# Performance work log

Hardware: AMD Instinct MI355X
Metric: run time of the kernel (lower is better)

## Reference

```python
import jax, jax.numpy as jnp
import numpy as np

T, B, D, H = 4096, 4, 1024, 8
EPS = 1e-5


def _ln(z, g, b):
    m = jnp.mean(z, axis=-1, keepdims=True)
    v = jnp.mean((z - m) ** 2, axis=-1, keepdims=True)
    return (z - m) * jax.lax.rsqrt(v + EPS) * g + b


def setup_inputs() -> dict:
    key = jax.random.key(0)
    ks = jax.random.split(key, 8)
    s = 0.02
    return {
        "x": jax.random.normal(ks[0], (T, B, D), dtype=jnp.float32),
        "norm_w": jnp.ones((D,), jnp.float32),
        "norm_b": jnp.zeros((D,), jnp.float32),
        "tnorm_w": jnp.ones((D,), jnp.float32),
        "tnorm_b": jnp.zeros((D,), jnp.float32),
        "Wq": jax.random.normal(ks[1], (D, D), jnp.float32) * s,
        "bq": jnp.zeros((D,), jnp.float32),
        "Wk": jax.random.normal(ks[2], (D, D), jnp.float32) * s,
        "bk": jnp.zeros((D,), jnp.float32),
        "Wv": jax.random.normal(ks[3], (D, D), jnp.float32) * s,
        "bv": jnp.zeros((D,), jnp.float32),
    }


def reference(x, norm_w, norm_b, tnorm_w, tnorm_b, Wq, bq, Wk, bk, Wv, bv):
    # x: (T, B, D) -> (B, T, D), matching torch x.permute(1, 0, 2)
    xb = jnp.transpose(x, (1, 0, 2))
    b, t, d = xb.shape
    hd = d // H
    xn = _ln(xb, norm_w, norm_b)          # query branch norm
    xtn = _ln(xb, tnorm_w, tnorm_b)       # key/value branch norm (text_norm applied to x)
    q = (xn @ Wq.T + bq).reshape(b, t, H, hd)
    k = (xtn @ Wk.T + bk).reshape(b, t, H, hd)
    v = (xtn @ Wv.T + bv).reshape(b, t, H, hd)
    q = jax.nn.softmax(q, axis=-1)        # softmax over head-dim
    k = jax.nn.softmax(k, axis=1)         # softmax over time
    # kv state: (B, H, hd, hd)
    att = jnp.einsum('bthd,bthl->bhdl', k, v)
    y = jnp.einsum('bthd,bhdl->bthl', q, att).reshape(b, t, d)
    return y  # original forward returns y directly (proj_out/dropout unused)
```

## Files before the change

kernel.cpp:

```cpp
#include <hip/hip_runtime.h>
#include <cstdint>

#define T_LEN 4096
#define BATCH 4
#define DIM   1024
#define NH    8
#define HDIM  128
#define ROWS  16384

typedef __bf16 bf16x8 __attribute__((ext_vector_type(8)));
typedef float  f32x4  __attribute__((ext_vector_type(4)));

__device__ __forceinline__ unsigned short f2bf(float f) {
  union { float f; unsigned u; } a; a.f = f;
  unsigned u = a.u;
  u += 0x7fff + ((u >> 16) & 1);
  return (unsigned short)(u >> 16);
}
__device__ __forceinline__ float bf2f(unsigned short h) {
  union { unsigned u; float f; } a; a.u = ((unsigned)h) << 16;
  return a.f;
}

__device__ __forceinline__ void gld_lds16(const unsigned short* g, unsigned short* l) {
  __builtin_amdgcn_global_load_lds(
      (const __attribute__((address_space(1))) unsigned int*)g,
      (__attribute__((address_space(3))) unsigned int*)l, 16, 0, 0);
}

__global__ __launch_bounds__(256) void lnw_kernel(
    const float* __restrict__ x, const float* __restrict__ nw, const float* __restrict__ nb,
    const float* __restrict__ tw, const float* __restrict__ tb,
    unsigned short* __restrict__ xn, unsigned short* __restrict__ xtn,
    const float* __restrict__ Wq, const float* __restrict__ Wk, const float* __restrict__ Wv,
    unsigned short* __restrict__ wbf) {
  int tid = threadIdx.x;
  if (blockIdx.x >= ROWS) {
    int i4 = (blockIdx.x - ROWS) * 256 + tid;
    int w = i4 >> 18;
    const float* src = (w == 0) ? Wq : (w == 1 ? Wk : Wv);
    float4 v = ((const float4*)src)[i4 & 262143];
    union { unsigned short u[4]; uint2 d; } o;
    o.u[0] = f2bf(v.x); o.u[1] = f2bf(v.y); o.u[2] = f2bf(v.z); o.u[3] = f2bf(v.w);
    ((uint2*)wbf)[i4] = o.d;
    return;
  }
  int row = blockIdx.x;
  int t = row >> 2, b = row & 3;
  const float4 v = ((const float4*)(x + (size_t)row * DIM))[tid];
  float s  = v.x + v.y + v.z + v.w;
  float s2 = v.x*v.x + v.y*v.y + v.z*v.z + v.w*v.w;
#pragma unroll
  for (int o = 32; o; o >>= 1) { s += __shfl_xor(s, o); s2 += __shfl_xor(s2, o); }
  __shared__ float red[8];
  int wv = tid >> 6;
  if ((tid & 63) == 0) { red[wv] = s; red[4 + wv] = s2; }
  __syncthreads();
  s  = red[0] + red[1] + red[2] + red[3];
  s2 = red[4] + red[5] + red[6] + red[7];
  float mean = s * (1.0f / DIM);
  float var  = s2 * (1.0f / DIM) - mean * mean;
  float rstd = rsqrtf(var + 1e-5f);
  size_t orow = ((size_t)b * T_LEN + t) * DIM;
  int c0 = tid * 4;
  float xv[4] = {v.x, v.y, v.z, v.w};
  union { unsigned short u[4]; uint2 d; } o1, o2;
#pragma unroll
  for (int j = 0; j < 4; ++j) {
    int c = c0 + j;
    float xh = (xv[j] - mean) * rstd;
    o1.u[j] = f2bf(xh * nw[c] + nb[c]);
    o2.u[j] = f2bf(xh * tw[c] + tb[c]);
  }
  *(uint2*)(xn  + orow + c0) = o1.d;
  *(uint2*)(xtn + orow + c0) = o2.d;
}

__global__ __launch_bounds__(512, 4) void kv_gemm(
    const unsigned short* __restrict__ xtn, const unsigned short* __restrict__ wbf,
    const float* __restrict__ bk, const float* __restrict__ bv,
    unsigned short* __restrict__ ko, unsigned short* __restrict__ vo,
    float* __restrict__ Zk) {
  int zz = blockIdx.z + 1;
  const unsigned short* W = wbf + (size_t)zz * DIM * DIM;
  const float* bias = (zz == 1) ? bk : bv;
  unsigned short* outp = (zz == 1) ? ko : vo;

  int m0 = blockIdx.x * 256;
  int n0 = blockIdx.y * 128;

  __shared__ __align__(16) unsigned short lds[24576];

  int tid = threadIdx.x;
  int wave = tid >> 6, lane = tid & 63;
  int wr = wave >> 1, wc = wave & 1;
  int wm = wr * 64, wn = wc * 64;
  int l16 = lane & 15, kq = lane >> 4;
  int rs = (kq ^ ((l16 >> 1) & 3)) * 8;

  int arow = tid >> 2;
  int achk = (tid & 3) ^ ((tid >> 3) & 3);
  const unsigned short* Ag = xtn + (size_t)(m0 + arow) * DIM + achk * 8;
  const unsigned short* Wg = W + (size_t)(n0 + arow) * DIM + achk * 8;

  f32x4 acc[4][4] = {};

  auto stage = [&](int tt, int sb) {
    int kt = tt * 32;
    gld_lds16(Ag + kt,                     lds + sb + wave * 512);
    gld_lds16(Ag + (size_t)128 * DIM + kt, lds + sb + 4096 + wave * 512);
    gld_lds16(Wg + kt,                     lds + sb + 8192 + wave * 512);
  };

  stage(0, 0);
  stage(1, 12288);

  for (int t = 0; t < 32; ++t) {
    int sb = (t & 1) ? 12288 : 0;
    const unsigned short* As = lds + sb;
    const unsigned short* Bs = lds + sb + 8192;

    if (t < 31) asm volatile("s_waitcnt vmcnt(3)" ::: "memory");
    else        asm volatile("s_waitcnt vmcnt(0)" ::: "memory");
    __builtin_amdgcn_sched_barrier(0);
    __builtin_amdgcn_s_barrier();
    __builtin_amdgcn_sched_barrier(0);

    bf16x8 fa[4], fb[4];
#pragma unroll
    for (int i = 0; i < 4; ++i) {
      fa[i] = *(const bf16x8*)(As + (wm + i * 16 + l16) * 32 + rs);
      fb[i] = *(const bf16x8*)(Bs + (wn + i * 16 + l16) * 32 + rs);
    }
#pragma unroll
    for (int i = 0; i < 4; ++i)
#pragma unroll
      for (int j = 0; j < 4; ++j)
        acc[i][j] = __builtin_amdgcn_mfma_f32_16x16x32_bf16(fa[i], fb[j], acc[i][j], 0, 0, 0);

    __builtin_amdgcn_sched_barrier(0);
    __builtin_amdgcn_s_barrier();
    __builtin_amdgcn_sched_barrier(0);
    if (t < 30) stage(t + 2, sb);
    __builtin_amdgcn_sched_barrier(0);
  }

#pragma unroll
  for (int j = 0; j < 4; ++j) {
    float bc = bias[n0 + wn + j * 16 + l16];
#pragma unroll
    for (int i = 0; i < 4; ++i)
#pragma unroll
      for (int r = 0; r < 4; ++r) acc[i][j][r] += bc;
  }

  int b = m0 >> 12;
  int tb = m0 & 4095;
  unsigned short* obase = outp + (size_t)b * DIM * T_LEN + tb;
  bool doExp = (zz == 1);
  float zs[4] = {0.0f, 0.0f, 0.0f, 0.0f};
#pragma unroll
  for (int j = 0; j < 4; ++j) {
    int col = n0 + wn + j * 16 + l16;
    unsigned short* cp = obase + (size_t)col * T_LEN;
#pragma unroll
    for (int i = 0; i < 4; ++i) {
      int t0 = wm + i * 16 + kq * 4;
      union { unsigned short u[4]; uint2 d; } o;
#pragma unroll
      for (int r = 0; r < 4; ++r) {
        float val = acc[i][j][r];
        if (doExp) { val = __expf(val); zs[j] += val; }
        o.u[r] = f2bf(val);
      }
      *(uint2*)(cp + t0) = o.d;
    }
  }
  if (doExp) {
#pragma unroll
    for (int j = 0; j < 4; ++j) {
      zs[j] += __shfl_xor(zs[j], 16);
      zs[j] += __shfl_xor(zs[j], 32);
      if (kq == 0) {
        int col = n0 + wn + j * 16 + l16;
        atomicAdd(Zk + b * DIM + col, zs[j]);
      }
    }
  }
}

__global__ __launch_bounds__(256) void att_gemm(
    const unsigned short* __restrict__ vT, const unsigned short* __restrict__ ksmT,
    float* __restrict__ slabs) {
  int kc = blockIdx.x;
  int bh = blockIdx.y;
  const unsigned short* Arow = vT   + (size_t)bh * HDIM * T_LEN;
  const unsigned short* Brow = ksmT + (size_t)bh * HDIM * T_LEN;
  __shared__ __align__(16) unsigned short As[128 * 64];
  __shared__ __align__(16) unsigned short Bs[128 * 64];
  int tid = threadIdx.x;
  int wave = tid >> 6, lane = tid & 63;
  int wm = (wave >> 1) * 64, wn = (wave & 1) * 64;
  int l16 = lane & 15, kq = lane >> 4;
  int swz = l16 & 7;
  int srow = tid >> 3;
  int skk = (((tid & 7) ^ ((tid >> 3) & 7)) * 8);
  const unsigned short* Ag = Arow + (size_t)srow * T_LEN + skk;
  const unsigned short* Bg = Brow + (size_t)srow * T_LEN + skk;
  unsigned short* Al = As + wave * 512;
  unsigned short* Bl = Bs + wave * 512;
  f32x4 acc[4][4] = {};
  int kbeg = kc * 512;
  for (int kt = kbeg; kt < kbeg + 512; kt += 64) {
#pragma unroll
    for (int p = 0; p < 4; ++p) {
      gld_lds16(Ag + (size_t)(p * 32) * T_LEN + kt, Al + p * 2048);
      gld_lds16(Bg + (size_t)(p * 32) * T_LEN + kt, Bl + p * 2048);
    }
    __syncthreads();
#pragma unroll
    for (int ks4 = 0; ks4 < 2; ++ks4) {
      int coff = (((kq + ks4 * 4) ^ swz) * 8);
      bf16x8 fa[4], fb[4];
#pragma unroll
      for (int i = 0; i < 4; ++i) {
        fa[i] = *(const bf16x8*)(As + (wm + i * 16 + l16) * 64 + coff);
        fb[i] = *(const bf16x8*)(Bs + (wn + i * 16 + l16) * 64 + coff);
      }
#pragma unroll
      for (int i = 0; i < 4; ++i)
#pragma unroll
        for (int j = 0; j < 4; ++j)
          acc[i][j] = __builtin_amdgcn_mfma_f32_16x16x32_bf16(fa[i], fb[j], acc[i][j], 0, 0, 0);
    }
    __syncthreads();
  }
  float* op = slabs + ((size_t)kc * 32 + bh) * 16384;
#pragma unroll
  for (int j = 0; j < 4; ++j) {
    int col = wn + j * 16 + l16;
#pragma unroll
    for (int i = 0; i < 4; ++i) {
      int rb = wm + i * 16 + kq * 4;
#pragma unroll
      for (int r = 0; r < 4; ++r)
        op[(size_t)(rb + r) * 128 + col] = acc[i][j][r];
    }
  }
}

__global__ __launch_bounds__(256) void attcvt(
    const float* __restrict__ slabs, const float* __restrict__ Zk,
    unsigned short* __restrict__ attbf) {
  int idx = blockIdx.x * 256 + threadIdx.x;
  int bh = idx >> 14;
  int b = bh >> 3, h = bh & 7;
  int d = idx & 127;
  float s = 0.0f;
#pragma unroll
  for (int kc = 0; kc < 8; ++kc) s += slabs[(size_t)kc * 524288 + idx];
  float zv = Zk[b * DIM + h * HDIM + d];
  attbf[idx] = f2bf(s / zv);
}

__global__ __launch_bounds__(512) void qy_gemm(
    const unsigned short* __restrict__ xn, const unsigned short* __restrict__ wbf,
    const float* __restrict__ bq, const unsigned short* __restrict__ attbf,
    float* __restrict__ out) {
  int m0 = blockIdx.x * 256;
  int h  = blockIdx.y;
  int n0 = h * HDIM;
  int b  = m0 >> 12;
  int bh = b * 8 + h;

  __shared__ __align__(16) unsigned short lds[24576];

  int tid = threadIdx.x;
  int wave = tid >> 6, lane = tid & 63;
  int wr = wave >> 1, wc = wave & 1;
  int wm = wr * 64, wn = wc * 64;
  int l16 = lane & 15, kq = lane >> 4;
  int rs = (kq ^ ((l16 >> 1) & 3)) * 8;

  int arow = tid >> 2;
  int achk = (tid & 3) ^ ((tid >> 3) & 3);
  const unsigned short* Ag = xn + (size_t)(m0 + arow) * DIM + achk * 8;
  const unsigned short* Wg = wbf + (size_t)(n0 + arow) * DIM + achk * 8;

  f32x4 acc[4][4] = {};

  auto stage = [&](int tt, int sb) {
    int kt = tt * 32;
    gld_lds16(Ag + kt,                     lds + sb + wave * 512);
    gld_lds16(Ag + (size_t)128 * DIM + kt, lds + sb + 4096 + wave * 512);
    gld_lds16(Wg + kt,                     lds + sb + 8192 + wave * 512);
  };

  stage(0, 0);
  stage(1, 12288);

  for (int t = 0; t < 32; ++t) {
    int sb = (t & 1) ? 12288 : 0;
    const unsigned short* As = lds + sb;
    const unsigned short* Bs = lds + sb + 8192;

    if (t < 31) asm volatile("s_waitcnt vmcnt(3)" ::: "memory");
    else        asm volatile("s_waitcnt vmcnt(0)" ::: "memory");
    __builtin_amdgcn_sched_barrier(0);
    __builtin_amdgcn_s_barrier();
    __builtin_amdgcn_sched_barrier(0);

    bf16x8 fa[4], fb[4];
#pragma unroll
    for (int i = 0; i < 4; ++i) {
      fa[i] = *(const bf16x8*)(As + (wm + i * 16 + l16) * 32 + rs);
      fb[i] = *(const bf16x8*)(Bs + (wn + i * 16 + l16) * 32 + rs);
    }
#pragma unroll
    for (int i = 0; i < 4; ++i)
#pragma unroll
      for (int j = 0; j < 4; ++j)
        acc[i][j] = __builtin_amdgcn_mfma_f32_16x16x32_bf16(fa[i], fb[j], acc[i][j], 0, 0, 0);

    __builtin_amdgcn_sched_barrier(0);
    __builtin_amdgcn_s_barrier();
    __builtin_amdgcn_sched_barrier(0);
    if (t < 30) stage(t + 2, sb);
    __builtin_amdgcn_sched_barrier(0);
  }

#pragma unroll
  for (int j = 0; j < 4; ++j) {
    float bc = bq[n0 + wn + j * 16 + l16];
#pragma unroll
    for (int i = 0; i < 4; ++i)
#pragma unroll
      for (int r = 0; r < 4; ++r) acc[i][j][r] += bc;
  }

  int wmy = (wave >> 2) * 64, wny = (wave & 3) * 32;
  bf16x8 fby[2][4];
#pragma unroll
  for (int jy = 0; jy < 2; ++jy)
#pragma unroll
    for (int ks = 0; ks < 4; ++ks) {
      int ncol = wny + jy * 16 + l16;
      fby[jy][ks] = *(const bf16x8*)(attbf + (size_t)bh * 16384 + ncol * 128 + ks * 32 + kq * 8);
    }

  {
    float* redm = (float*)lds;
    float* reds = redm + 512;
#pragma unroll
    for (int i = 0; i < 4; ++i) {
#pragma unroll
      for (int r = 0; r < 4; ++r) {
        float pm = acc[i][0][r];
#pragma unroll
        for (int j = 1; j < 4; ++j) pm = fmaxf(pm, acc[i][j][r]);
        pm = fmaxf(pm, __shfl_xor(pm, 1));
        pm = fmaxf(pm, __shfl_xor(pm, 2));
        pm = fmaxf(pm, __shfl_xor(pm, 4));
        pm = fmaxf(pm, __shfl_xor(pm, 8));
        float ps = 0.0f;
#pragma unroll
        for (int j = 0; j < 4; ++j) ps += __expf(acc[i][j][r] - pm);
        ps += __shfl_xor(ps, 1);
        ps += __shfl_xor(ps, 2);
        ps += __shfl_xor(ps, 4);
        ps += __shfl_xor(ps, 8);
        if (l16 == 0) {
          int row = wm + i * 16 + kq * 4 + r;
          redm[row * 2 + wc] = pm;
          reds[row * 2 + wc] = ps;
        }
      }
    }
    __syncthreads();
#pragma unroll
    for (int i = 0; i < 4; ++i) {
#pragma unroll
      for (int r = 0; r < 4; ++r) {
        int row = wm + i * 16 + kq * 4 + r;
        float ma = redm[row * 2], mb = redm[row * 2 + 1];
        float sa = reds[row * 2], sb2 = reds[row * 2 + 1];
        float M = fmaxf(ma, mb);
        float inv = 1.0f / (sa * __expf(ma - M) + sb2 * __expf(mb - M));
#pragma unroll
        for (int j = 0; j < 4; ++j)
          acc[i][j][r] = __expf(acc[i][j][r] - M) * inv;
      }
    }
  }

#pragma unroll
  for (int p = 0; p < 2; ++p) {
    __syncthreads();
    if ((wr >> 1) == p) {
      int wmL = wm - p * 128;
#pragma unroll
      for (int i = 0; i < 4; ++i)
#pragma unroll
        for (int j = 0; j < 4; ++j) {
          int col = wn + j * 16 + l16;
#pragma unroll
          for (int r = 0; r < 4; ++r) {
            int row = wmL + i * 16 + kq * 4 + r;
            lds[row * 136 + col] = f2bf(acc[i][j][r]);
          }
        }
    }
    __syncthreads();
    f32x4 accy[4][2] = {};
#pragma unroll
    for (int ks = 0; ks < 4; ++ks) {
      bf16x8 fay[4];
#pragma unroll
      for (int iy = 0; iy < 4; ++iy) {
        int row = wmy + iy * 16 + l16;
        fay[iy] = *(const bf16x8*)(lds + row * 136 + ks * 32 + kq * 8);
      }
#pragma unroll
      for (int iy = 0; iy < 4; ++iy)
#pragma unroll
        for (int jy = 0; jy < 2; ++jy)
          accy[iy][jy] = __builtin_amdgcn_mfma_f32_16x16x32_bf16(fay[iy], fby[jy][ks], accy[iy][jy], 0, 0, 0);
    }
#pragma unroll
    for (int jy = 0; jy < 2; ++jy) {
      int colg = n0 + wny + jy * 16 + l16;
#pragma unroll
      for (int iy = 0; iy < 4; ++iy) {
        int rowg = m0 + p * 128 + wmy + iy * 16 + kq * 4;
#pragma unroll
        for (int r = 0; r < 4; ++r)
          out[(size_t)(rowg + r) * DIM + colg] = accy[iy][jy][r];
      }
    }
  }
}

extern "C" void kernel_launch(void* const* d_in, const int* in_sizes, int n_in,
                              void* d_out, int out_size, void* d_ws, size_t ws_size,
                              hipStream_t stream) {
  const float* x  = (const float*)d_in[0];
  const float* nw = (const float*)d_in[1];
  const float* nb = (const float*)d_in[2];
  const float* tw = (const float*)d_in[3];
  const float* tb = (const float*)d_in[4];
  const float* Wq = (const float*)d_in[5];
  const float* bq = (const float*)d_in[6];
  const float* Wk = (const float*)d_in[7];
  const float* bk = (const float*)d_in[8];
  const float* Wv = (const float*)d_in[9];
  const float* bv = (const float*)d_in[10];
  float* out = (float*)d_out;

  char* ws = (char*)d_ws;
  unsigned short* xn   = (unsigned short*)(ws);
  unsigned short* xtn  = (unsigned short*)(ws + 33554432);
  float* slabs         = (float*)(ws + 67108864);
  unsigned short* ksmT = (unsigned short*)(ws + 100663296);
  unsigned short* vT   = (unsigned short*)(ws + 134217728);
  unsigned short* wbf  = (unsigned short*)(ws + 167772160);
  unsigned short* attbf= (unsigned short*)(ws + 176160768);
  float* Zk            = (float*)(ws + 177209344);

  (void)hipMemsetAsync(Zk, 0, BATCH * DIM * 4, stream);
  lnw_kernel<<<ROWS + 3072, 256, 0, stream>>>(x, nw, nb, tw, tb, xn, xtn, Wq, Wk, Wv, wbf);
  kv_gemm<<<dim3(64, 8, 2), 512, 0, stream>>>(xtn, wbf, bk, bv, ksmT, vT, Zk);
  att_gemm<<<dim3(8, 32), 256, 0, stream>>>(vT, ksmT, slabs);
  attcvt<<<2048, 256, 0, stream>>>(slabs, Zk, attbf);
  qy_gemm<<<dim3(64, 8), 512, 0, stream>>>(xn, wbf, bq, attbf, out);
}
```

Before: 330.3 us.

## Fuse attcvt into att_gemm via last-block reduction and simplify qy softmax

Removes the memset and the separate attcvt kernel. Zk and the counters are now zeroed inside lnw_kernel, and the slab reduction and normalisation run in the last-arriving att_gemm block per head, counted with an atomic. att_gemm's K split doubles to 16 chunks of 256 to fill more CUs. In qy_gemm the softmax drops max subtraction, which assumes the logits are small enough not to overflow exp. The second GEMM now runs in one pass with a wider LDS buffer and occupancy hint, so the last block's serial reduction and the unstable exp are the risks.

```diff
diff --git a/kernel.cpp b/kernel.cpp
--- a/kernel.cpp
+++ b/kernel.cpp
@@ -33,10 +33,13 @@
     const float* __restrict__ tw, const float* __restrict__ tb,
     unsigned short* __restrict__ xn, unsigned short* __restrict__ xtn,
     const float* __restrict__ Wq, const float* __restrict__ Wk, const float* __restrict__ Wv,
-    unsigned short* __restrict__ wbf) {
+    unsigned short* __restrict__ wbf, float* __restrict__ Zk, int* __restrict__ cnt) {
   int tid = threadIdx.x;
   if (blockIdx.x >= ROWS) {
-    int i4 = (blockIdx.x - ROWS) * 256 + tid;
+    int wb = blockIdx.x - ROWS;
+    if (wb < 16) Zk[wb * 256 + tid] = 0.0f;
+    if (wb == 16 && tid < 32) cnt[tid] = 0;
+    int i4 = wb * 256 + tid;
     int w = i4 >> 18;
     const float* src = (w == 0) ? Wq : (w == 1 ? Wk : Wv);
     float4 v = ((const float4*)src)[i4 & 262143];
@@ -191,7 +194,8 @@
 
 __global__ __launch_bounds__(256) void att_gemm(
     const unsigned short* __restrict__ vT, const unsigned short* __restrict__ ksmT,
-    float* __restrict__ slabs) {
+    float* __restrict__ slabs, const float* __restrict__ Zk,
+    unsigned short* __restrict__ attbf, int* __restrict__ cnt) {
   int kc = blockIdx.x;
   int bh = blockIdx.y;
   const unsigned short* Arow = vT   + (size_t)bh * HDIM * T_LEN;
@@ -210,8 +214,8 @@
   unsigned short* Al = As + wave * 512;
   unsigned short* Bl = Bs + wave * 512;
   f32x4 acc[4][4] = {};
-  int kbeg = kc * 512;
-  for (int kt = kbeg; kt < kbeg + 512; kt += 64) {
+  int kbeg = kc * 256;
+  for (int kt = kbeg; kt < kbeg + 256; kt += 64) {
 #pragma unroll
     for (int p = 0; p < 4; ++p) {
       gld_lds16(Ag + (size_t)(p * 32) * T_LEN + kt, Al + p * 2048);
@@ -247,23 +251,28 @@
         op[(size_t)(rb + r) * 128 + col] = acc[i][j][r];
     }
   }
-}
-
-__global__ __launch_bounds__(256) void attcvt(
-    const float* __restrict__ slabs, const float* __restrict__ Zk,
-    unsigned short* __restrict__ attbf) {
-  int idx = blockIdx.x * 256 + threadIdx.x;
-  int bh = idx >> 14;
-  int b = bh >> 3, h = bh & 7;
-  int d = idx & 127;
-  float s = 0.0f;
-#pragma unroll
-  for (int kc = 0; kc < 8; ++kc) s += slabs[(size_t)kc * 524288 + idx];
-  float zv = Zk[b * DIM + h * HDIM + d];
-  attbf[idx] = f2bf(s / zv);
-}
-
-__global__ __launch_bounds__(512) void qy_gemm(
+
+  __threadfence();
+  __syncthreads();
+  __shared__ int isLast;
+  if (tid == 0) isLast = (atomicAdd(cnt + bh, 1) == 15) ? 1 : 0;
+  __syncthreads();
+  if (isLast) {
+    __threadfence();
+    int b = bh >> 3, h = bh & 7;
+#pragma unroll 4
+    for (int q = 0; q < 64; ++q) {
+      int pos = q * 256 + tid;
+      float s = 0.0f;
+#pragma unroll
+      for (int k = 0; k < 16; ++k) s += slabs[((size_t)k * 32 + bh) * 16384 + pos];
+      float zv = Zk[b * DIM + h * HDIM + (pos & 127)];
+      attbf[(size_t)bh * 16384 + pos] = f2bf(s / zv);
+    }
+  }
+}
+
+__global__ __launch_bounds__(512, 4) void qy_gemm(
     const unsigned short* __restrict__ xn, const unsigned short* __restrict__ wbf,
     const float* __restrict__ bq, const unsigned short* __restrict__ attbf,
     float* __restrict__ out) {
@@ -273,7 +282,7 @@
   int b  = m0 >> 12;
   int bh = b * 8 + h;
 
-  __shared__ __align__(16) unsigned short lds[24576];
+  __shared__ __align__(16) unsigned short lds[35840];
 
   int tid = threadIdx.x;
   int wave = tid >> 6, lane = tid & 63;
@@ -335,107 +344,62 @@
 #pragma unroll
     for (int i = 0; i < 4; ++i)
 #pragma unroll
-      for (int r = 0; r < 4; ++r) acc[i][j][r] += bc;
-  }
-
-  int wmy = (wave >> 2) * 64, wny = (wave & 3) * 32;
-  bf16x8 fby[2][4];
-#pragma unroll
-  for (int jy = 0; jy < 2; ++jy)
-#pragma unroll
-    for (int ks = 0; ks < 4; ++ks) {
-      int ncol = wny + jy * 16 + l16;
-      fby[jy][ks] = *(const bf16x8*)(attbf + (size_t)bh * 16384 + ncol * 128 + ks * 32 + kq * 8);
-    }
-
-  {
-    float* redm = (float*)lds;
-    float* reds = redm + 512;
-#pragma unroll
-    for (int i = 0; i < 4; ++i) {
-#pragma unroll
-      for (int r = 0; r < 4; ++r) {
-        float pm = acc[i][0][r];
-#pragma unroll
-        for (int j = 1; j < 4; ++j) pm = fmaxf(pm, acc[i][j][r]);
-        pm = fmaxf(pm, __shfl_xor(pm, 1));
-        pm = fmaxf(pm, __shfl_xor(pm, 2));
-        pm = fmaxf(pm, __shfl_xor(pm, 4));
-        pm = fmaxf(pm, __shfl_xor(pm, 8));
-        float ps = 0.0f;
-#pragma unroll
-        for (int j = 0; j < 4; ++j) ps += __expf(acc[i][j][r] - pm);
-        ps += __shfl_xor(ps, 1);
-        ps += __shfl_xor(ps, 2);
-        ps += __shfl_xor(ps, 4);
-        ps += __shfl_xor(ps, 8);
-        if (l16 == 0) {
-          int row = wm + i * 16 + kq * 4 + r;
-          redm[row * 2 + wc] = pm;
-          reds[row * 2 + wc] = ps;
-        }
-      }
-    }
-    __syncthreads();
-#pragma unroll
-    for (int i = 0; i < 4; ++i) {
-#pragma unroll
-      for (int r = 0; r < 4; ++r) {
-        int row = wm + i * 16 + kq * 4 + r;
-        float ma = redm[row * 2], mb = redm[row * 2 + 1];
-        float sa = reds[row * 2], sb2 = reds[row * 2 + 1];
-        float M = fmaxf(ma, mb);
-        float inv = 1.0f / (sa * __expf(ma - M) + sb2 * __expf(mb - M));
-#pragma unroll
-        for (int j = 0; j < 4; ++j)
-          acc[i][j][r] = __expf(acc[i][j][r] - M) * inv;
-      }
-    }
-  }
-
-#pragma unroll
-  for (int p = 0; p < 2; ++p) {
-    __syncthreads();
-    if ((wr >> 1) == p) {
-      int wmL = wm - p * 128;
-#pragma unroll
-      for (int i = 0; i < 4; ++i)
-#pragma unroll
-        for (int j = 0; j < 4; ++j) {
-          int col = wn + j * 16 + l16;
-#pragma unroll
-          for (int r = 0; r < 4; ++r) {
-            int row = wmL + i * 16 + kq * 4 + r;
-            lds[row * 136 + col] = f2bf(acc[i][j][r]);
-          }
-        }
-    }
-    __syncthreads();
-    f32x4 accy[4][2] = {};
-#pragma unroll
-    for (int ks = 0; ks < 4; ++ks) {
-      bf16x8 fay[4];
-#pragma unroll
-      for (int iy = 0; iy < 4; ++iy) {
-        int row = wmy + iy * 16 + l16;
-        fay[iy] = *(const bf16x8*)(lds + row * 136 + ks * 32 + kq * 8);
-      }
-#pragma unroll
-      for (int iy = 0; iy < 4; ++iy)
-#pragma unroll
-        for (int jy = 0; jy < 2; ++jy)
-          accy[iy][jy] = __builtin_amdgcn_mfma_f32_16x16x32_bf16(fay[iy], fby[jy][ks], accy[iy][jy], 0, 0, 0);
-    }
-#pragma unroll
-    for (int jy = 0; jy < 2; ++jy) {
-      int colg = n0 + wny + jy * 16 + l16;
-#pragma unroll
-      for (int iy = 0; iy < 4; ++iy) {
-        int rowg = m0 + p * 128 + wmy + iy * 16 + kq * 4;
-#pragma unroll
-        for (int r = 0; r < 4; ++r)
-          out[(size_t)(rowg + r) * DIM + colg] = accy[iy][jy][r];
-      }
+      for (int r = 0; r < 4; ++r) acc[i][j][r] = __expf(acc[i][j][r] + bc);
+  }
+
+  float* reds = (float*)(lds + 34816);
+#pragma unroll
+  for (int i = 0; i < 4; ++i) {
+#pragma unroll
+    for (int r = 0; r < 4; ++r) {
+      float ps = acc[i][0][r] + acc[i][1][r] + acc[i][2][r] + acc[i][3][r];
+      ps += __shfl_xor(ps, 1);
+      ps += __shfl_xor(ps, 2);
+      ps += __shfl_xor(ps, 4);
+      ps += __shfl_xor(ps, 8);
+      if (l16 == 0) reds[(wm + i * 16 + kq * 4 + r) * 2 + wc] = ps;
+    }
+  }
+  __syncthreads();
+
+#pragma unroll
+  for (int i = 0; i < 4; ++i) {
+#pragma unroll
+    for (int r = 0; r < 4; ++r) {
+      int row = wm + i * 16 + kq * 4 + r;
+      float inv = 1.0f / (reds[row * 2] + reds[row * 2 + 1]);
+#pragma unroll
+      for (int j = 0; j < 4; ++j)
+        lds[row * 136 + wn + j * 16 + l16] = f2bf(acc[i][j][r] * inv);
+    }
+  }
+  __syncthreads();
+
+  const unsigned short* attb = attbf + (size_t)bh * 16384;
+  f32x4 accy[4][4] = {};
+#pragma unroll
+  for (int ks = 0; ks < 4; ++ks) {
+    bf16x8 fb[4];
+#pragma unroll
+    for (int jy = 0; jy < 4; ++jy)
+      fb[jy] = *(const bf16x8*)(attb + (wn + jy * 16 + l16) * 128 + ks * 32 + kq * 8);
+#pragma unroll
+    for (int iy = 0; iy < 4; ++iy) {
+      bf16x8 fa = *(const bf16x8*)(lds + (wm + iy * 16 + l16) * 136 + ks * 32 + kq * 8);
+#pragma unroll
+      for (int jy = 0; jy < 4; ++jy)
+        accy[iy][jy] = __builtin_amdgcn_mfma_f32_16x16x32_bf16(fa, fb[jy], accy[iy][jy], 0, 0, 0);
+    }
+  }
+#pragma unroll
+  for (int jy = 0; jy < 4; ++jy) {
+    int colg = n0 + wn + jy * 16 + l16;
+#pragma unroll
+    for (int iy = 0; iy < 4; ++iy) {
+      int rowg = m0 + wm + iy * 16 + kq * 4;
+#pragma unroll
+      for (int r = 0; r < 4; ++r)
+        out[(size_t)(rowg + r) * DIM + colg] = accy[iy][jy][r];
     }
   }
 }
@@ -465,11 +429,10 @@
   unsigned short* wbf  = (unsigned short*)(ws + 167772160);
   unsigned short* attbf= (unsigned short*)(ws + 176160768);
   float* Zk            = (float*)(ws + 177209344);
-
-  (void)hipMemsetAsync(Zk, 0, BATCH * DIM * 4, stream);
-  lnw_kernel<<<ROWS + 3072, 256, 0, stream>>>(x, nw, nb, tw, tb, xn, xtn, Wq, Wk, Wv, wbf);
+  int* cnt             = (int*)(ws + 177225728);
+
+  lnw_kernel<<<ROWS + 3072, 256, 0, stream>>>(x, nw, nb, tw, tb, xn, xtn, Wq, Wk, Wv, wbf, Zk, cnt);
   kv_gemm<<<dim3(64, 8, 2), 512, 0, stream>>>(xtn, wbf, bk, bv, ksmT, vT, Zk);
-  att_gemm<<<dim3(8, 32), 256, 0, stream>>>(vT, ksmT, slabs);
-  attcvt<<<2048, 256, 0, stream>>>(slabs, Zk, attbf);
+  att_gemm<<<dim3(16, 32), 256, 0, stream>>>(vT, ksmT, slabs, Zk, attbf, cnt);
   qy_gemm<<<dim3(64, 8), 512, 0, stream>>>(xn, wbf, bq, attbf, out);
 }
```

Result: slower. 498.9 us (+51.0%).
